# Optimization experiments

Measured on AMD Instinct MI355X. Metric: run time of the kernel, lower is better.

Reference implementation:

```python
import jax, jax.numpy as jnp
import numpy as np

EPS_BN = 1e-5
EPS_LN = 1e-5

def _gelu(x):
    return jax.nn.gelu(x, approximate=False)  # torch nn.GELU default is erf-based

def _conv(x, w, b, stride):
    y = jax.lax.conv_general_dilated(x, w, (stride, stride), 'VALID',
                                     dimension_numbers=('NCHW', 'OIHW', 'NCHW'))
    return y + b[None, :, None, None]

def _bn_train(x, g, b):
    # training-mode BatchNorm2d: batch statistics over (N,H,W), biased variance
    m = x.mean(axis=(0, 2, 3), keepdims=True)
    v = ((x - m) ** 2).mean(axis=(0, 2, 3), keepdims=True)
    return g[None, :, None, None] * (x - m) * jax.lax.rsqrt(v + EPS_BN) + b[None, :, None, None]

def _ln(x, g, b):
    m = x.mean(-1, keepdims=True)
    v = ((x - m) ** 2).mean(-1, keepdims=True)
    return g * (x - m) * jax.lax.rsqrt(v + EPS_LN) + b

def setup_inputs() -> dict:
    key = jax.random.key(0)
    ks = jax.random.split(key, 16)
    B, E, D, H = 1024, 8, 256, 512
    cnn_out = 128 * 14 * 16  # 28672
    s = 0.02
    inp = {
        'x': jax.random.normal(ks[0], (B, 4, 144, 160), jnp.float32),
        'conv1_w': jax.random.normal(ks[1], (32, 4, 8, 8), jnp.float32) * s,
        'conv1_b': jnp.zeros((32,), jnp.float32),
        'bn1_g': jnp.ones((32,), jnp.float32), 'bn1_b': jnp.zeros((32,), jnp.float32),
        'conv2_w': jax.random.normal(ks[2], (64, 32, 4, 4), jnp.float32) * s,
        'conv2_b': jnp.zeros((64,), jnp.float32),
        'bn2_g': jnp.ones((64,), jnp.float32), 'bn2_b': jnp.zeros((64,), jnp.float32),
        'conv3_w': jax.random.normal(ks[3], (128, 64, 3, 3), jnp.float32) * s,
        'conv3_b': jnp.zeros((128,), jnp.float32),
        'bn3_g': jnp.ones((128,), jnp.float32), 'bn3_b': jnp.zeros((128,), jnp.float32),
        'proj_w': jax.random.normal(ks[4], (D, cnn_out), jnp.float32) * 0.005,
        'proj_b': jnp.zeros((D,), jnp.float32),
        'ln_g': jnp.ones((D,), jnp.float32), 'ln_b': jnp.zeros((D,), jnp.float32),
        'router_w': jax.random.normal(ks[5], (E, D), jnp.float32) * 0.01,
        'expert_bias': jnp.zeros((E,), jnp.float32),
        'ew1': jax.random.normal(ks[6], (E, H, D), jnp.float32) * s,
        'eb1': jnp.zeros((E, H), jnp.float32),
        'ew2': jax.random.normal(ks[7], (E, D, H), jnp.float32) * s,
        'eb2': jnp.zeros((E, D), jnp.float32),
        'sw1': jax.random.normal(ks[8], (D, D), jnp.float32) * s,  # shared expert hidden = 512//2 = 256
        'sb1': jnp.zeros((D,), jnp.float32),
        'sw2': jax.random.normal(ks[9], (D, D), jnp.float32) * s,
        'sb2': jnp.zeros((D,), jnp.float32),
        'moe_ln_g': jnp.ones((D,), jnp.float32), 'moe_ln_b': jnp.zeros((D,), jnp.float32),
    }
    return inp

def reference(x, conv1_w, conv1_b, bn1_g, bn1_b, conv2_w, conv2_b, bn2_g, bn2_b,
              conv3_w, conv3_b, bn3_g, bn3_b, proj_w, proj_b, ln_g, ln_b,
              router_w, expert_bias, ew1, eb1, ew2, eb2, sw1, sb1, sw2, sb2,
              moe_ln_g, moe_ln_b):
    B = x.shape[0]
    E = router_w.shape[0]
    top_k = 2
    # conv backbone
    h = _gelu(_bn_train(_conv(x, conv1_w, conv1_b, 4), bn1_g, bn1_b))
    h = _gelu(_bn_train(_conv(h, conv2_w, conv2_b, 2), bn2_g, bn2_b))
    h = _gelu(_bn_train(_conv(h, conv3_w, conv3_b, 1), bn3_g, bn3_b))
    h = h.reshape(B, -1)  # [B, 128*14*16]
    # projection
    h = _gelu(_ln(h @ proj_w.T + proj_b, ln_g, ln_b))  # [B, 256]
    # router (eval: no noise)
    logits = h @ router_w.T + expert_bias          # [B, E]
    probs = jax.nn.softmax(logits, axis=-1)
    wts, idx = jax.lax.top_k(probs, top_k)          # [B, k]
    wts = wts / (wts.sum(-1, keepdims=True) + 1e-8)
    # dense expert compute, sparse combine (same math as masked dispatch loop)
    hid = _gelu(jnp.einsum('bd,ehd->beh', h, ew1) + eb1)   # [B, E, 512]
    eout = jnp.einsum('beh,edh->bed', hid, ew2) + eb2       # [B, E, 256]
    combine = jnp.zeros((B, E), h.dtype).at[jnp.arange(B)[:, None], idx].add(wts)
    out = jnp.einsum('be,bed->bd', combine, eout)
    # shared expert
    shared = _gelu(h @ sw1.T + sb1) @ sw2.T + sb2
    out = out + 0.5 * shared
    # aux losses
    pm = probs.mean(0)
    lb_loss = ((pm - 1.0 / E) ** 2).sum() * E
    z_loss = (logits ** 2).mean() * 0.001
    out = _ln(out, moe_ln_g, moe_ln_b)
    return out, lb_loss, z_loss
```

## Files before the change

kernel.cpp:

```cpp
#include <hip/hip_runtime.h>
#include <hip/hip_bf16.h>
#include <math.h>

typedef unsigned short u16;
typedef unsigned int u32;
typedef __attribute__((ext_vector_type(8))) short bf16x8;
typedef __attribute__((ext_vector_type(4))) float f32x4;

#define DEV __device__ __forceinline__

DEV float gelu_f(float x) { return 0.5f * x * (1.0f + erff(x * 0.70710678118654752f)); }
DEV u16 f2bf(float f) { u32 u = __builtin_bit_cast(u32, f); u = (u + 0x7FFFu + ((u >> 16) & 1u)) >> 16; return (u16)u; }
DEV float bf2f(u16 h) { return __builtin_bit_cast(float, (u32)h << 16); }
DEV u32 fbits(float f) { return __builtin_bit_cast(u32, f); }
DEV float ubits(u32 u) { return __builtin_bit_cast(float, u); }
DEV u32 psplit(float v) {
  u32 u = fbits(v);
  float lo = v - ubits(u & 0xFFFF0000u);
  return (u >> 16) | (fbits(lo) & 0xFFFF0000u);
}
DEV float punp(u32 p) { return ubits(p << 16) + ubits(p & 0xFFFF0000u); }
DEV f32x4 mfma3(bf16x8 ah, bf16x8 al, bf16x8 bh, bf16x8 bl, f32x4 c) {
  c = __builtin_amdgcn_mfma_f32_16x16x32_bf16(al, bh, c, 0, 0, 0);
  c = __builtin_amdgcn_mfma_f32_16x16x32_bf16(ah, bl, c, 0, 0, 0);
  c = __builtin_amdgcn_mfma_f32_16x16x32_bf16(ah, bh, c, 0, 0, 0);
  return c;
}

__global__ void k_zero(float* p, int n) {
  int i = blockIdx.x * blockDim.x + threadIdx.x;
  if (i < n) p[i] = 0.f;
}

__global__ void k_wprep1(const float* __restrict__ w, u16* __restrict__ wh, u16* __restrict__ wl) {
  int idx = blockIdx.x * 256 + threadIdx.x; if (idx >= 8192) return;
  int j = idx & 7, lane = (idx >> 3) & 63, s = (idx >> 9) & 7, oct = idx >> 12;
  int oc = oct * 16 + (lane & 15);
  int kl = ((lane >> 4) << 3) + j;
  int kw = kl >> 2, c = kl & 3, kh = s;
  float v = w[((oc * 4 + c) * 8 + kh) * 8 + kw];
  u16 h = f2bf(v); wh[idx] = h; wl[idx] = f2bf(v - bf2f(h));
}
__global__ void k_wprep2(const float* __restrict__ w, u16* __restrict__ wh, u16* __restrict__ wl) {
  int idx = blockIdx.x * 256 + threadIdx.x; if (idx >= 32768) return;
  int j = idx & 7, lane = (idx >> 3) & 63, s = (idx >> 9) & 15, oct = idx >> 13;
  int oc = oct * 16 + (lane & 15);
  int k = s * 32 + ((lane >> 4) << 3) + j;
  int kh = k >> 7, kw = (k >> 5) & 3, c = k & 31;
  float v = w[((oc * 32 + c) * 4 + kh) * 4 + kw];
  u16 h = f2bf(v); wh[idx] = h; wl[idx] = f2bf(v - bf2f(h));
}
__global__ void k_wprep3(const float* __restrict__ w, u16* __restrict__ wh, u16* __restrict__ wl) {
  int idx = blockIdx.x * 256 + threadIdx.x; if (idx >= 73728) return;
  int j = idx & 7, lane = (idx >> 3) & 63, rest = idx >> 9;
  int s = rest % 18, oct = rest / 18;
  int oc = oct * 16 + (lane & 15);
  int k = s * 32 + ((lane >> 4) << 3) + j;
  int kh = k / 192, r = k - kh * 192;
  int kw = r >> 6, c = r & 63;
  float v = w[((oc * 64 + c) * 3 + kh) * 3 + kw];
  u16 h = f2bf(v); wh[idx] = h; wl[idx] = f2bf(v - bf2f(h));
}
__global__ __launch_bounds__(256) void k_wprepP(const float* __restrict__ w,
    u16* __restrict__ wh, u16* __restrict__ wl)
{
  __shared__ float tile[16][4][225];
  int q = blockIdx.x, oct = blockIdx.y, tid = threadIdx.x;
  for (int i = tid; i < 3584; i += 256) {
    int n = i / 224, rem = i % 224, e = rem / 56, f4 = rem % 56;
    float4 v = *(const float4*)(w + (long)(oct * 16 + n) * 28672 + (4 * q + e) * 224 + f4 * 4);
    tile[n][e][f4 * 4 + 0] = v.x; tile[n][e][f4 * 4 + 1] = v.y;
    tile[n][e][f4 * 4 + 2] = v.z; tile[n][e][f4 * 4 + 3] = v.w;
  }
  __syncthreads();
  int g = (q >> 1) & 3, j0 = 4 * (q & 1), sgb = q >> 3;
  for (int o = tid; o < 3584; o += 256) {
    int pix = o >> 4, ln = o & 15;
    u16 hs[4], ls[4];
#pragma unroll
    for (int e = 0; e < 4; ++e) {
      float v = tile[ln][e][pix];
      u16 h = f2bf(v); hs[e] = h; ls[e] = f2bf(v - bf2f(h));
    }
    long base = (((long)oct * 896 + pix * 4 + sgb) * 64 + g * 16 + ln) * 8 + j0;
    *(uint2*)(wh + base) = make_uint2((u32)hs[0] | ((u32)hs[1] << 16), (u32)hs[2] | ((u32)hs[3] << 16));
    *(uint2*)(wl + base) = make_uint2((u32)ls[0] | ((u32)ls[1] << 16), (u32)ls[2] | ((u32)ls[3] << 16));
  }
}
__global__ void k_wprepG(const float* __restrict__ w, u16* __restrict__ wf,
                         int N, int K, long total)
{
  long idx = (long)blockIdx.x * 256 + threadIdx.x; if (idx >= total) return;
  int j = (int)(idx & 7); int lane = (int)((idx >> 3) & 63); long rest = idx >> 9;
  int kn = K >> 5;
  int s = (int)(rest % kn); long rest2 = rest / kn;
  int noct = N >> 4;
  int oct = (int)(rest2 % noct); int z = (int)(rest2 / noct);
  int n = oct * 16 + (lane & 15);
  int k = s * 32 + ((lane >> 4) << 3) + j;
  wf[idx] = f2bf(w[((long)z * N + n) * K + k]);
}

DEV void c1_store(u16* sin0, u16* sin1, int i, float4 v0, float4 v1) {
  const float* a0 = (const float*)&v0;
  const float* a1 = (const float*)&v1;
  int cp = i / 800, rem = i - cp * 800, r = rem / 40, q = rem - r * 40;
#pragma unroll
  for (int m = 0; m < 4; ++m) {
    float f0 = a0[m], f1 = a1[m];
    u32 u0 = fbits(f0), u1 = fbits(f1);
    u32 hh = (u0 >> 16) | (u1 & 0xFFFF0000u);
    float l0 = f0 - ubits(u0 & 0xFFFF0000u);
    float l1 = f1 - ubits(u1 & 0xFFFF0000u);
    u32 ll = (fbits(l0) >> 16) | (fbits(l1) & 0xFFFF0000u);
    int col = q * 4 + m;
    int idx = r * 320 + col * 2 + cp;
    idx ^= ((col >> 4) & 3) << 2;
    ((u32*)sin0)[idx] = hh;
    ((u32*)sin1)[idx] = ll;
  }
}

__global__ __launch_bounds__(256, 3) void k_conv1m(const float* __restrict__ x,
    const u16* __restrict__ wfh, const u16* __restrict__ wfl,
    const float* __restrict__ bias, u32* __restrict__ y1p, float* __restrict__ sums)
{
  __shared__ __align__(16) u16 sin0[12800], sin1[12800];
  __shared__ float bs1[32], bs2[32];
  int ohp = blockIdx.x, b = blockIdx.y, tid = threadIdx.x;
  int row0 = ohp * 16;
  if (tid < 32) { bs1[tid] = 0.f; bs2[tid] = 0.f; }
  {
    float4 v0r[6], v1r[6];
#pragma unroll
    for (int it = 0; it < 6; ++it) {
      int i = tid + it * 256;
      int cp = i / 800, rem = i - cp * 800, r = rem / 40, q = rem - r * 40;
      int grow = row0 + r;
      float4 z = make_float4(0.f, 0.f, 0.f, 0.f);
      v0r[it] = z; v1r[it] = z;
      if (grow < 144) {
        long base = ((long)b * 4 + 2 * cp) * 23040 + (long)grow * 160 + q * 4;
        v0r[it] = *(const float4*)(x + base);
        v1r[it] = *(const float4*)(x + base + 23040);
      }
    }
#pragma unroll
    for (int it = 0; it < 6; ++it)
      c1_store(sin0, sin1, tid + it * 256, v0r[it], v1r[it]);
    if (tid < 64) {
      int i = 1536 + tid;
      int cp = i / 800, rem = i - cp * 800, r = rem / 40, q = rem - r * 40;
      int grow = row0 + r;
      float4 v0 = make_float4(0.f, 0.f, 0.f, 0.f), v1 = v0;
      if (grow < 144) {
        long base = ((long)b * 4 + 2 * cp) * 23040 + (long)grow * 160 + q * 4;
        v0 = *(const float4*)(x + base);
        v1 = *(const float4*)(x + base + 23040);
      }
      c1_store(sin0, sin1, i, v0, v1);
    }
  }
  __syncthreads();
  int w = tid >> 6, lane = tid & 63, g = lane >> 4, ln = lane & 15;
  int ohls[3], owcs[3];
#pragma unroll
  for (int jj = 0; jj < 3; ++jj) {
    int j = w + 4 * jj;
    ohls[jj] = j / 3;
    int owc = (j % 3) * 16 + ln; if (owc > 38) owc = 38;
    owcs[jj] = owc;
  }
  f32x4 z4 = {0.f, 0.f, 0.f, 0.f};
  f32x4 acc[3][2];
#pragma unroll
  for (int jj = 0; jj < 3; ++jj) { acc[jj][0] = z4; acc[jj][1] = z4; }
#pragma unroll
  for (int kh = 0; kh < 8; ++kh) {
    bf16x8 bh0 = *(const bf16x8*)&wfh[kh * 512 + lane * 8];
    bf16x8 bl0 = *(const bf16x8*)&wfl[kh * 512 + lane * 8];
    bf16x8 bh1 = *(const bf16x8*)&wfh[4096 + kh * 512 + lane * 8];
    bf16x8 bl1 = *(const bf16x8*)&wfl[4096 + kh * 512 + lane * 8];
#pragma unroll
    for (int jj = 0; jj < 3; ++jj) {
      int col = owcs[jj] * 4 + g * 2;
      int off = (4 * ohls[jj] + kh) * 640 + col * 4;
      off ^= ((col >> 4) & 3) << 3;
      bf16x8 ah = *(const bf16x8*)&sin0[off];
      bf16x8 al = *(const bf16x8*)&sin1[off];
      acc[jj][0] = mfma3(ah, al, bh0, bl0, acc[jj][0]);
      acc[jj][1] = mfma3(ah, al, bh1, bl1, acc[jj][1]);
    }
  }
  float s1[2] = {0.f, 0.f}, s2[2] = {0.f, 0.f};
#pragma unroll
  for (int jj = 0; jj < 3; ++jj) {
    int j = w + 4 * jj;
    int ohl = j / 3, owt = j % 3;
    int oh = 4 * ohp + ohl;
    if (oh >= 35) continue;
#pragma unroll
    for (int oct = 0; oct < 2; ++oct) {
      int oc = oct * 16 + ln;
      float bv = bias[oc];
#pragma unroll
      for (int r = 0; r < 4; ++r) {
        int owo = owt * 16 + g * 4 + r;
        if (owo < 39) {
          long oi = ((long)b * 1365 + oh * 39 + owo) * 32 + oc;
          float v = acc[jj][oct][r] + bv;
          y1p[oi] = psplit(v);
          s1[oct] += v; s2[oct] += v * v;
        }
      }
    }
  }
#pragma unroll
  for (int o = 16; o <= 32; o <<= 1) {
    s1[0] += __shfl_xor(s1[0], o); s1[1] += __shfl_xor(s1[1], o);
    s2[0] += __shfl_xor(s2[0], o); s2[1] += __shfl_xor(s2[1], o);
  }
  if (g == 0) {
    atomicAdd(&bs1[ln], s1[0]); atomicAdd(&bs1[16 + ln], s1[1]);
    atomicAdd(&bs2[ln], s2[0]); atomicAdd(&bs2[16 + ln], s2[1]);
  }
  __syncthreads();
  int bkt = b & 7;
  if (tid < 32) {
    atomicAdd(&sums[bkt * 64 + tid], bs1[tid]);
    atomicAdd(&sums[bkt * 64 + 32 + tid], bs2[tid]);
  }
}

DEV void bn_store(u16* sin0, u16* sin1, int i, uint4 p4, int cbmask,
                  const float* sc, const float* shf) {
  int cb = (i & cbmask) * 4;
  u32 hw[2], lw[2];
  u32 pe[4] = { p4.x, p4.y, p4.z, p4.w };
#pragma unroll
  for (int half = 0; half < 2; ++half) {
    float va = punp(pe[half * 2 + 0]);
    float vb = punp(pe[half * 2 + 1]);
    float aa = gelu_f(va * sc[cb + half * 2 + 0] + shf[cb + half * 2 + 0]);
    float ab = gelu_f(vb * sc[cb + half * 2 + 1] + shf[cb + half * 2 + 1]);
    u32 ua = fbits(aa), ub = fbits(ab);
    float la = aa - ubits(ua & 0xFFFF0000u);
    float lb = ab - ubits(ub & 0xFFFF0000u);
    hw[half] = (ua >> 16) | (ub & 0xFFFF0000u);
    lw[half] = (fbits(la) >> 16) | (fbits(lb) & 0xFFFF0000u);
  }
  int iw = i ^ (((i >> 4) & 7) << 1);
  ((uint2*)sin0)[iw] = make_uint2(hw[0], hw[1]);
  ((uint2*)sin1)[iw] = make_uint2(lw[0], lw[1]);
}

__global__ __launch_bounds__(256, 3) void k_conv2m(const u32* __restrict__ y1p,
    const u16* __restrict__ wfh, const u16* __restrict__ wfl,
    const float* __restrict__ scale, const float* __restrict__ shift,
    const float* __restrict__ bias, u32* __restrict__ y2p, float* __restrict__ sums)
{
  __shared__ __align__(16) u16 sin0[12480], sin1[12480];
  __shared__ float sc[32], shf[32];
  __shared__ float bs1[64], bs2[64];
  int ohq = blockIdx.x, b = blockIdx.y, tid = threadIdx.x;
  if (tid < 32) { sc[tid] = scale[tid]; shf[tid] = shift[tid]; }
  if (tid < 64) { bs1[tid] = 0.f; bs2[tid] = 0.f; }
  __syncthreads();
  long sb = ((long)b * 1365 + (long)ohq * 312) * 32;
  const uint4* srcP = (const uint4*)(y1p + sb);
  {
    uint4 pr[12];
#pragma unroll
    for (int it = 0; it < 12; ++it) pr[it] = srcP[tid + it * 256];
#pragma unroll
    for (int it = 0; it < 12; ++it) bn_store(sin0, sin1, tid + it * 256, pr[it], 7, sc, shf);
    if (tid < 48) {
      int i = 3072 + tid;
      bn_store(sin0, sin1, i, srcP[i], 7, sc, shf);
    }
  }
  __syncthreads();
  int w = tid >> 6, lane = tid & 63, g = lane >> 4, ln = lane & 15;
  int oct = w;
  int rowb[5], colb[5];
#pragma unroll
  for (int j = 0; j < 5; ++j) {
    int p = j * 16 + ln; if (p > 71) p = 71;
    int ohl = p / 18, ow = p - 18 * ohl;
    rowb[j] = 2 * ohl; colb[j] = 2 * ow;
  }
  f32x4 z4 = {0.f, 0.f, 0.f, 0.f};
  f32x4 acc[5];
#pragma unroll
  for (int j = 0; j < 5; ++j) acc[j] = z4;
#pragma unroll
  for (int s = 0; s < 16; ++s) {
    int kh = s >> 2, kw = s & 3;
    bf16x8 bh = *(const bf16x8*)&wfh[oct * 8192 + s * 512 + lane * 8];
    bf16x8 bl = *(const bf16x8*)&wfl[oct * 8192 + s * 512 + lane * 8];
#pragma unroll
    for (int j = 0; j < 5; ++j) {
      int colpix = (rowb[j] + kh) * 39 + colb[j] + kw;
      int off = colpix * 32 + g * 8;
      off ^= ((colpix >> 1) & 7) << 3;
      bf16x8 ah = *(const bf16x8*)&sin0[off];
      bf16x8 al = *(const bf16x8*)&sin1[off];
      acc[j] = mfma3(ah, al, bh, bl, acc[j]);
    }
  }
  int oc = oct * 16 + ln;
  float bv = bias[oc];
  float s1 = 0.f, s2 = 0.f;
#pragma unroll
  for (int j = 0; j < 5; ++j) {
#pragma unroll
    for (int r = 0; r < 4; ++r) {
      int po = j * 16 + g * 4 + r;
      if (po < 72) {
        long oi = ((long)b * 288 + (long)ohq * 72 + po) * 64 + oc;
        float v = acc[j][r] + bv;
        y2p[oi] = psplit(v);
        s1 += v; s2 += v * v;
      }
    }
  }
#pragma unroll
  for (int o = 16; o <= 32; o <<= 1) { s1 += __shfl_xor(s1, o); s2 += __shfl_xor(s2, o); }
  if (g == 0) { atomicAdd(&bs1[oc], s1); atomicAdd(&bs2[oc], s2); }
  __syncthreads();
  int bkt = b & 7;
  if (tid < 64) {
    atomicAdd(&sums[bkt * 128 + tid], bs1[tid]);
    atomicAdd(&sums[bkt * 128 + 64 + tid], bs2[tid]);
  }
}

__global__ __launch_bounds__(256, 3) void k_conv3m(const u32* __restrict__ y2p,
    const u16* __restrict__ wfh, const u16* __restrict__ wfl,
    const float* __restrict__ scale, const float* __restrict__ shift,
    const float* __restrict__ bias, u32* __restrict__ y3p, float* __restrict__ sums)
{
  __shared__ __align__(16) u16 sin0[10368], sin1[10368];
  __shared__ float sc[64], shf[64];
  __shared__ float bs1[128], bs2[128];
  int hh = blockIdx.x, b = blockIdx.y, tid = threadIdx.x;
  if (tid < 64) { sc[tid] = scale[tid]; shf[tid] = shift[tid]; }
  if (tid < 128) { bs1[tid] = 0.f; bs2[tid] = 0.f; }
  __syncthreads();
  long sb = ((long)b * 288 + (long)hh * 126) * 64;
  const uint4* srcP = (const uint4*)(y2p + sb);
  {
    uint4 pr[10];
#pragma unroll
    for (int it = 0; it < 10; ++it) pr[it] = srcP[tid + it * 256];
#pragma unroll
    for (int it = 0; it < 10; ++it) bn_store(sin0, sin1, tid + it * 256, pr[it], 15, sc, shf);
    if (tid < 32) {
      int i = 2560 + tid;
      bn_store(sin0, sin1, i, srcP[i], 15, sc, shf);
    }
  }
  __syncthreads();
  int w = tid >> 6, lane = tid & 63, g = lane >> 4, ln = lane & 15;
  int oct0 = w * 2;
  f32x4 z4 = {0.f, 0.f, 0.f, 0.f};
  f32x4 acc[7][2];
#pragma unroll
  for (int j = 0; j < 7; ++j) { acc[j][0] = z4; acc[j][1] = z4; }
#pragma unroll 6
  for (int s = 0; s < 18; ++s) {
    const int kh = s / 6, rm = s % 6;
    const int kw = rm >> 1, ch = rm & 1;
    bf16x8 bh0 = *(const bf16x8*)&wfh[oct0 * 9216 + s * 512 + lane * 8];
    bf16x8 bl0 = *(const bf16x8*)&wfl[oct0 * 9216 + s * 512 + lane * 8];
    bf16x8 bh1 = *(const bf16x8*)&wfh[(oct0 + 1) * 9216 + s * 512 + lane * 8];
    bf16x8 bl1 = *(const bf16x8*)&wfl[(oct0 + 1) * 9216 + s * 512 + lane * 8];
#pragma unroll
    for (int j = 0; j < 7; ++j) {
      int colpix = (j + kh) * 18 + ln + kw;
      int off = colpix * 64 + ch * 32 + g * 8;
      off ^= (colpix & 7) << 3;
      bf16x8 ah = *(const bf16x8*)&sin0[off];
      bf16x8 al = *(const bf16x8*)&sin1[off];
      acc[j][0] = mfma3(ah, al, bh0, bl0, acc[j][0]);
      acc[j][1] = mfma3(ah, al, bh1, bl1, acc[j][1]);
    }
  }
  float s1[2] = {0.f, 0.f}, s2[2] = {0.f, 0.f};
#pragma unroll
  for (int j = 0; j < 7; ++j) {
#pragma unroll
    for (int o2 = 0; o2 < 2; ++o2) {
      int oc = (oct0 + o2) * 16 + ln;
      float bv = bias[oc];
#pragma unroll
      for (int r = 0; r < 4; ++r) {
        int owo = g * 4 + r;
        long oi = ((long)b * 224 + (hh * 7 + j) * 16 + owo) * 128 + oc;
        float v = acc[j][o2][r] + bv;
        y3p[oi] = psplit(v);
        s1[o2] += v; s2[o2] += v * v;
      }
    }
  }
#pragma unroll
  for (int o = 16; o <= 32; o <<= 1) {
    s1[0] += __shfl_xor(s1[0], o); s1[1] += __shfl_xor(s1[1], o);
    s2[0] += __shfl_xor(s2[0], o); s2[1] += __shfl_xor(s2[1], o);
  }
  if (g == 0) {
    atomicAdd(&bs1[oct0 * 16 + ln], s1[0]); atomicAdd(&bs1[(oct0 + 1) * 16 + ln], s1[1]);
    atomicAdd(&bs2[oct0 * 16 + ln], s2[0]); atomicAdd(&bs2[(oct0 + 1) * 16 + ln], s2[1]);
  }
  __syncthreads();
  int bkt = b & 7;
  if (tid < 128) {
    atomicAdd(&sums[bkt * 256 + tid], bs1[tid]);
    atomicAdd(&sums[bkt * 256 + 128 + tid], bs2[tid]);
  }
}

__global__ void k_bn_finalize(const float* __restrict__ sums, const float* __restrict__ g,
    const float* __restrict__ b, float* __restrict__ scale, float* __restrict__ shift,
    int C, float invN)
{
  int c = threadIdx.x;
  if (c < C) {
    float s1 = 0.f, s2 = 0.f;
#pragma unroll
    for (int k = 0; k < 8; ++k) {
      s1 += sums[k * 2 * C + c];
      s2 += sums[k * 2 * C + C + c];
    }
    float m = s1 * invN;
    float var = s2 * invN - m * m;
    float sc = g[c] * rsqrtf(var + 1e-5f);
    scale[c] = sc;
    shift[c] = b[c] - m * sc;
  }
}

__global__ __launch_bounds__(256, 2) void k_projm(const u32* __restrict__ y3p,
    const u16* __restrict__ bh_g, const u16* __restrict__ bl_g,
    const float* __restrict__ scale, const float* __restrict__ shift,
    float* __restrict__ part)
{
  __shared__ __align__(16) u16 Ah[4096], Al[4096];
  __shared__ __align__(16) u16 Bh[8192], Bl[8192];
  __shared__ float sc3[128], sh3[128];
  int m0 = blockIdx.x * 128, by = blockIdx.y, tid = threadIdx.x;
  int w = tid >> 6, lane = tid & 63, g = lane >> 4, ln = lane & 15;
  if (tid < 128) { sc3[tid] = scale[tid]; sh3[tid] = shift[tid]; }
  f32x4 z4 = {0.f, 0.f, 0.f, 0.f};
  f32x4 acc[2][16];
#pragma unroll
  for (int p = 0; p < 2; ++p)
#pragma unroll
    for (int o = 0; o < 16; ++o) acc[p][o] = z4;
  for (int ks = 0; ks < 28; ++ks) {
    __syncthreads();
    long k0 = ((long)by * 28 + ks) * 32;
    int cbase = (int)(k0 & 127);
#pragma unroll
    for (int ii = 0; ii < 4; ++ii) {
      int i = tid + ii * 256;
      int row = i >> 3, q = i & 7;
      uint4 p4 = *((const uint4*)(y3p + (long)(m0 + row) * 28672 + k0) + q);
      u32 pe[4] = { p4.x, p4.y, p4.z, p4.w };
      int c0 = cbase + q * 4;
      u16 hs[4], ls[4];
#pragma unroll
      for (int j = 0; j < 4; ++j) {
        float v = punp(pe[j]);
        float a = gelu_f(v * sc3[c0 + j] + sh3[c0 + j]);
        u32 ua = fbits(a);
        float la = a - ubits(ua & 0xFFFF0000u);
        hs[j] = (u16)(ua >> 16);
        ls[j] = (u16)(fbits(la) >> 16);
      }
      ((uint2*)Ah)[i] = make_uint2((u32)hs[0] | ((u32)hs[1] << 16), (u32)hs[2] | ((u32)hs[3] << 16));
      ((uint2*)Al)[i] = make_uint2((u32)ls[0] | ((u32)ls[1] << 16), (u32)ls[2] | ((u32)ls[3] << 16));
    }
    int ksg = by * 28 + ks;
#pragma unroll
    for (int ii = 0; ii < 8; ++ii) {
      int i = tid + ii * 256;
      int arr = i >> 10, idx = i & 1023, oct = idx >> 6, r2 = idx & 63;
      const u16* src = arr ? bl_g : bh_g;
      u16* dst = arr ? Bl : Bh;
      ((uint4*)dst)[idx] = *((const uint4*)(src + ((long)oct * 896 + ksg) * 512) + r2);
    }
    __syncthreads();
    bf16x8 a_h[2], a_l[2];
#pragma unroll
    for (int pt = 0; pt < 2; ++pt) {
      int off = ((2 * w + pt) * 16 + ln) * 32 + g * 8;
      a_h[pt] = *(const bf16x8*)&Ah[off];
      a_l[pt] = *(const bf16x8*)&Al[off];
    }
#pragma unroll
    for (int oct = 0; oct < 16; ++oct) {
      bf16x8 bh = *(const bf16x8*)&Bh[oct * 512 + lane * 8];
      bf16x8 bl = *(const bf16x8*)&Bl[oct * 512 + lane * 8];
#pragma unroll
      for (int pt = 0; pt < 2; ++pt)
        acc[pt][oct] = mfma3(a_h[pt], a_l[pt], bh, bl, acc[pt][oct]);
    }
  }
#pragma unroll
  for (int pt = 0; pt < 2; ++pt)
#pragma unroll
    for (int oct = 0; oct < 16; ++oct) {
      int oc = oct * 16 + ln;
#pragma unroll
      for (int r = 0; r < 4; ++r) {
        int tok = m0 + (2 * w + pt) * 16 + g * 4 + r;
        part[((long)by * 1024 + tok) * 256 + oc] = acc[pt][oct][r];
      }
    }
}

__global__ __launch_bounds__(256) void k_lnred(const float* __restrict__ part,
    const float* __restrict__ pb, const float* __restrict__ g, const float* __restrict__ be,
    float* __restrict__ h, u16* __restrict__ hb)
{
  int b = blockIdx.x, d = threadIdx.x;
  float s = pb[d];
#pragma unroll
  for (int ks = 0; ks < 32; ++ks) s += part[((long)ks * 1024 + b) * 256 + d];
  __shared__ float red[4];
  float t = s;
  for (int o = 32; o; o >>= 1) t += __shfl_xor(t, o);
  if ((d & 63) == 0) red[d >> 6] = t;
  __syncthreads();
  float mean = (red[0] + red[1] + red[2] + red[3]) * (1.f / 256.f);
  __syncthreads();
  float dv = s - mean;
  t = dv * dv;
  for (int o = 32; o; o >>= 1) t += __shfl_xor(t, o);
  if ((d & 63) == 0) red[d >> 6] = t;
  __syncthreads();
  float var = (red[0] + red[1] + red[2] + red[3]) * (1.f / 256.f);
  float hv = gelu_f(g[d] * dv * rsqrtf(var + 1e-5f) + be[d]);
  h[b * 256 + d] = hv;
  hb[b * 256 + d] = f2bf(hv);
}

__global__ __launch_bounds__(256, 2) void k_gemmb(const u16* __restrict__ A, long aZ, int K,
    const u16* __restrict__ Bf, int noct_tot,
    const float* __restrict__ bias, int biasZ,
    void* __restrict__ C, long cZ, int ldc, int outbf, int act)
{
  __shared__ __align__(16) u16 As[2048];
  __shared__ __align__(16) u16 Bs[8192];
  int m0 = blockIdx.x * 64, nb = blockIdx.y, z = blockIdx.z, tid = threadIdx.x;
  int w = tid >> 6, lane = tid & 63, g = lane >> 4, ln = lane & 15;
  const u16* Az = A + (long)z * aZ;
  int kn = K >> 5;
  f32x4 z4 = {0.f, 0.f, 0.f, 0.f};
  f32x4 acc[16];
#pragma unroll
  for (int o = 0; o < 16; ++o) acc[o] = z4;
  for (int ks = 0; ks < kn; ++ks) {
    __syncthreads();
    {
      int row = tid >> 2, q = tid & 3;
      ((uint4*)As)[tid] = *((const uint4*)(Az + (long)(m0 + row) * K + ks * 32) + q);
    }
#pragma unroll
    for (int ii = 0; ii < 4; ++ii) {
      int i = tid + ii * 256;
      int oct = i >> 6, r2 = i & 63;
      const u16* src = Bf + (((long)z * noct_tot + nb * 16 + oct) * kn + ks) * 512;
      ((uint4*)Bs)[i] = ((const uint4*)src)[r2];
    }
    __syncthreads();
    bf16x8 a = *(const bf16x8*)&As[(w * 16 + ln) * 32 + g * 8];
#pragma unroll
    for (int oct = 0; oct < 16; ++oct) {
      bf16x8 bb = *(const bf16x8*)&Bs[oct * 512 + lane * 8];
      acc[oct] = __builtin_amdgcn_mfma_f32_16x16x32_bf16(a, bb, acc[oct], 0, 0, 0);
    }
  }
#pragma unroll
  for (int oct = 0; oct < 16; ++oct) {
    int n = nb * 256 + oct * 16 + ln;
    float bv = bias[z * biasZ + n];
#pragma unroll
    for (int r = 0; r < 4; ++r) {
      int tok = m0 + w * 16 + g * 4 + r;
      float v = acc[oct][r] + bv;
      if (act) v = gelu_f(v);
      long off = (long)z * cZ + (long)tok * ldc + n;
      if (outbf) ((u16*)C)[off] = f2bf(v);
      else ((float*)C)[off] = v;
    }
  }
}

__global__ __launch_bounds__(64) void k_router(const float* __restrict__ h,
    const float* __restrict__ rw, const float* __restrict__ eb,
    float* __restrict__ wts, int* __restrict__ idx,
    float* __restrict__ pm_sum, float* __restrict__ z_sum)
{
  int b = blockIdx.x, lane = threadIdx.x;
  float4 hv = *(const float4*)(h + b * 256 + lane * 4);
  float logit[8];
#pragma unroll
  for (int e = 0; e < 8; ++e) {
    float4 wv = *(const float4*)(rw + e * 256 + lane * 4);
    float p = hv.x * wv.x + hv.y * wv.y + hv.z * wv.z + hv.w * wv.w;
    for (int o = 32; o; o >>= 1) p += __shfl_xor(p, o);
    logit[e] = p + eb[e];
  }
  float mx = logit[0];
#pragma unroll
  for (int e = 1; e < 8; ++e) mx = fmaxf(mx, logit[e]);
  float pr[8]; float se = 0.f;
#pragma unroll
  for (int e = 0; e < 8; ++e) { pr[e] = expf(logit[e] - mx); se += pr[e]; }
  float inv = 1.f / se;
#pragma unroll
  for (int e = 0; e < 8; ++e) pr[e] *= inv;
  int i0 = 0; float v0 = pr[0];
#pragma unroll
  for (int e = 1; e < 8; ++e) if (pr[e] > v0) { v0 = pr[e]; i0 = e; }
  int i1 = -1; float v1 = -1.f;
#pragma unroll
  for (int e = 0; e < 8; ++e) if (e != i0 && pr[e] > v1) { v1 = pr[e]; i1 = e; }
  if (lane == 0) {
    float ssum = v0 + v1 + 1e-8f;
    wts[2 * b] = v0 / ssum; wts[2 * b + 1] = v1 / ssum;
    idx[2 * b] = i0; idx[2 * b + 1] = i1;
    float zz = 0.f;
#pragma unroll
    for (int e = 0; e < 8; ++e) zz += logit[e] * logit[e];
    atomicAdd(z_sum, zz);
  }
  if (lane < 8) atomicAdd(&pm_sum[lane], pr[lane]);
}

__global__ __launch_bounds__(256) void k_combine_ln(const float* __restrict__ eout,
    const float* __restrict__ sharedB, const float* __restrict__ wts, const int* __restrict__ idx,
    const float* __restrict__ g, const float* __restrict__ bb, float* __restrict__ out)
{
  int b = blockIdx.x, d = threadIdx.x;
  float w0 = wts[2 * b], w1 = wts[2 * b + 1];
  int i0 = idx[2 * b], i1 = idx[2 * b + 1];
  float val = w0 * eout[(long)i0 * 262144 + b * 256 + d]
            + w1 * eout[(long)i1 * 262144 + b * 256 + d]
            + 0.5f * sharedB[b * 256 + d];
  __shared__ float red[4];
  float s = val;
  for (int o = 32; o; o >>= 1) s += __shfl_xor(s, o);
  if ((d & 63) == 0) red[d >> 6] = s;
  __syncthreads();
  float mean = (red[0] + red[1] + red[2] + red[3]) * (1.f / 256.f);
  __syncthreads();
  float dv = val - mean;
  s = dv * dv;
  for (int o = 32; o; o >>= 1) s += __shfl_xor(s, o);
  if ((d & 63) == 0) red[d >> 6] = s;
  __syncthreads();
  float var = (red[0] + red[1] + red[2] + red[3]) * (1.f / 256.f);
  out[b * 256 + d] = g[d] * dv * rsqrtf(var + 1e-5f) + bb[d];
}

__global__ void k_losses(const float* __restrict__ pm_sum, const float* __restrict__ z_sum,
                         float* __restrict__ out)
{
  if (threadIdx.x == 0 && blockIdx.x == 0) {
    float lb = 0.f;
    for (int e = 0; e < 8; ++e) {
      float pm = pm_sum[e] * (1.f / 1024.f);
      float dd = pm - 0.125f;
      lb += dd * dd;
    }
    out[262144] = lb * 8.f;
    out[262145] = z_sum[0] * (1.f / 8192.f) * 0.001f;
  }
}

extern "C" void kernel_launch(void* const* d_in, const int* in_sizes, int n_in,
                              void* d_out, int out_size, void* d_ws, size_t ws_size,
                              hipStream_t stream)
{
  const float* x     = (const float*)d_in[0];
  const float* c1w   = (const float*)d_in[1];
  const float* c1b   = (const float*)d_in[2];
  const float* bn1g  = (const float*)d_in[3];
  const float* bn1b  = (const float*)d_in[4];
  const float* c2w   = (const float*)d_in[5];
  const float* c2b   = (const float*)d_in[6];
  const float* bn2g  = (const float*)d_in[7];
  const float* bn2b  = (const float*)d_in[8];
  const float* c3w   = (const float*)d_in[9];
  const float* c3b   = (const float*)d_in[10];
  const float* bn3g  = (const float*)d_in[11];
  const float* bn3b  = (const float*)d_in[12];
  const float* projw = (const float*)d_in[13];
  const float* projb = (const float*)d_in[14];
  const float* lng   = (const float*)d_in[15];
  const float* lnb   = (const float*)d_in[16];
  const float* rw    = (const float*)d_in[17];
  const float* ebias = (const float*)d_in[18];
  const float* ew1   = (const float*)d_in[19];
  const float* eb1   = (const float*)d_in[20];
  const float* ew2   = (const float*)d_in[21];
  const float* eb2   = (const float*)d_in[22];
  const float* sw1   = (const float*)d_in[23];
  const float* sb1   = (const float*)d_in[24];
  const float* sw2   = (const float*)d_in[25];
  const float* sb2   = (const float*)d_in[26];
  const float* mlng  = (const float*)d_in[27];
  const float* mlnb  = (const float*)d_in[28];
  float* out = (float*)d_out;

  char* W = (char*)d_ws;
  u32* y1p = (u32*)(W + 0);
  u32* y2p = (u32*)(W + 178913280L);
  u32* y3p = (u32*)(W + 0);
  u16* wfph = (u16*)(W + 254410752L);
  u16* wfpl = (u16*)(W + 269090816L);
  u16* wf1h = (u16*)(W + 283770880L);
  u16* wf1l = (u16*)(W + 283787264L);
  u16* wf2h = (u16*)(W + 283803648L);
  u16* wf2l = (u16*)(W + 283869184L);
  u16* wf3h = (u16*)(W + 283934720L);
  u16* wf3l = (u16*)(W + 284082176L);
  float* stats = (float*)(W + 284229632L);
  float* wtsb  = (float*)(W + 284246016L);
  int*   idxb  = (int*)(W + 284254208L);
  float* hbuf  = (float*)(W + 284262400L);
  float* shB   = (float*)(W + 286359552L);
  float* part  = (float*)(W + 178913280L);
  u16* hid     = (u16*)(W + 212467712L);
  u16* ewf1    = (u16*)(W + 220856320L);
  u16* ewf2    = (u16*)(W + 222953472L);
  u16* swf1    = (u16*)(W + 225050624L);
  u16* swf2    = (u16*)(W + 225181696L);
  float* eoutB = (float*)(W + 225312768L);
  u16* hbufb   = (u16*)(W + 233701376L);
  u16* sh1b    = (u16*)(W + 234225664L);

  float* sums1 = stats;
  float* sums2 = stats + 512;
  float* sums3 = stats + 1536;
  float* scale1 = stats + 3584; float* shift1 = stats + 3616;
  float* scale2 = stats + 3648; float* shift2 = stats + 3712;
  float* scale3 = stats + 3776; float* shift3 = stats + 3904;
  float* pm    = stats + 4032;  float* zsum  = stats + 4040;

  dim3 blk(256);
  k_zero<<<dim3(16), blk, 0, stream>>>(stats, 4096);
  k_wprep1<<<dim3(32), blk, 0, stream>>>(c1w, wf1h, wf1l);
  k_wprep2<<<dim3(128), blk, 0, stream>>>(c2w, wf2h, wf2l);
  k_wprep3<<<dim3(288), blk, 0, stream>>>(c3w, wf3h, wf3l);
  k_wprepP<<<dim3(32, 16), blk, 0, stream>>>(projw, wfph, wfpl);

  k_conv1m<<<dim3(9, 1024), blk, 0, stream>>>(x, wf1h, wf1l, c1b, y1p, sums1);
  k_bn_finalize<<<1, 32, 0, stream>>>(sums1, bn1g, bn1b, scale1, shift1, 32, 1.f / 1397760.f);

  k_conv2m<<<dim3(4, 1024), blk, 0, stream>>>(y1p, wf2h, wf2l, scale1, shift1, c2b, y2p, sums2);
  k_bn_finalize<<<1, 64, 0, stream>>>(sums2, bn2g, bn2b, scale2, shift2, 64, 1.f / 294912.f);

  k_conv3m<<<dim3(2, 1024), blk, 0, stream>>>(y2p, wf3h, wf3l, scale2, shift2, c3b, y3p, sums3);
  k_bn_finalize<<<1, 128, 0, stream>>>(sums3, bn3g, bn3b, scale3, shift3, 128, 1.f / 229376.f);

  k_wprepG<<<dim3(4096), blk, 0, stream>>>(ew1, ewf1, 512, 256, 1048576L);
  k_wprepG<<<dim3(4096), blk, 0, stream>>>(ew2, ewf2, 256, 512, 1048576L);
  k_wprepG<<<dim3(256), blk, 0, stream>>>(sw1, swf1, 256, 256, 65536L);
  k_wprepG<<<dim3(256), blk, 0, stream>>>(sw2, swf2, 256, 256, 65536L);

  k_projm<<<dim3(8, 32), blk, 0, stream>>>(y3p, wfph, wfpl, scale3, shift3, part);
  k_lnred<<<dim3(1024), blk, 0, stream>>>(part, projb, lng, lnb, hbuf, hbufb);

  k_router<<<dim3(1024), dim3(64), 0, stream>>>(hbuf, rw, ebias, wtsb, idxb, pm, zsum);

  k_gemmb<<<dim3(16, 2, 8), blk, 0, stream>>>(hbufb, 0L, 256, ewf1, 32, eb1, 512,
                                              (void*)hid, 524288L, 512, 1, 1);
  k_gemmb<<<dim3(16, 1, 8), blk, 0, stream>>>(hid, 524288L, 512, ewf2, 16, eb2, 256,
                                              (void*)eoutB, 262144L, 256, 0, 0);
  k_gemmb<<<dim3(16, 1, 1), blk, 0, stream>>>(hbufb, 0L, 256, swf1, 16, sb1, 0,
                                              (void*)sh1b, 0L, 256, 1, 1);
  k_gemmb<<<dim3(16, 1, 1), blk, 0, stream>>>(sh1b, 0L, 256, swf2, 16, sb2, 0,
                                              (void*)shB, 0L, 256, 0, 0);

  k_combine_ln<<<dim3(1024), blk, 0, stream>>>(eoutB, shB, wtsb, idxb, mlng, mlnb, out);
  k_losses<<<1, 64, 0, stream>>>(pm, zsum, out);
}
```

Before: 712.7 us.

## Merge prep kernels, fold BN finalize into consumers, fuse router and losses

Folds the stats zeroing and all the conv and expert weight-prep kernels into one launch. BN finalize now runs inside each consuming conv or projection block, the router is computed inside the LN-reduce kernel, and the loss kernel is merged into combine_ln. The point is to cut many small kernel launches and the tiny serial gaps between them. In exchange, every block redoes the BN finalize work. The loss tail in combine_ln now reads pm/z sums written by a previous kernel, which stays correct because of stream ordering.

```diff
diff --git a/kernel.cpp b/kernel.cpp
--- a/kernel.cpp
+++ b/kernel.cpp
@@ -26,71 +26,8 @@
   c = __builtin_amdgcn_mfma_f32_16x16x32_bf16(ah, bh, c, 0, 0, 0);
   return c;
 }
-
-__global__ void k_zero(float* p, int n) {
-  int i = blockIdx.x * blockDim.x + threadIdx.x;
-  if (i < n) p[i] = 0.f;
-}
-
-__global__ void k_wprep1(const float* __restrict__ w, u16* __restrict__ wh, u16* __restrict__ wl) {
-  int idx = blockIdx.x * 256 + threadIdx.x; if (idx >= 8192) return;
-  int j = idx & 7, lane = (idx >> 3) & 63, s = (idx >> 9) & 7, oct = idx >> 12;
-  int oc = oct * 16 + (lane & 15);
-  int kl = ((lane >> 4) << 3) + j;
-  int kw = kl >> 2, c = kl & 3, kh = s;
-  float v = w[((oc * 4 + c) * 8 + kh) * 8 + kw];
-  u16 h = f2bf(v); wh[idx] = h; wl[idx] = f2bf(v - bf2f(h));
-}
-__global__ void k_wprep2(const float* __restrict__ w, u16* __restrict__ wh, u16* __restrict__ wl) {
-  int idx = blockIdx.x * 256 + threadIdx.x; if (idx >= 32768) return;
-  int j = idx & 7, lane = (idx >> 3) & 63, s = (idx >> 9) & 15, oct = idx >> 13;
-  int oc = oct * 16 + (lane & 15);
-  int k = s * 32 + ((lane >> 4) << 3) + j;
-  int kh = k >> 7, kw = (k >> 5) & 3, c = k & 31;
-  float v = w[((oc * 32 + c) * 4 + kh) * 4 + kw];
-  u16 h = f2bf(v); wh[idx] = h; wl[idx] = f2bf(v - bf2f(h));
-}
-__global__ void k_wprep3(const float* __restrict__ w, u16* __restrict__ wh, u16* __restrict__ wl) {
-  int idx = blockIdx.x * 256 + threadIdx.x; if (idx >= 73728) return;
-  int j = idx & 7, lane = (idx >> 3) & 63, rest = idx >> 9;
-  int s = rest % 18, oct = rest / 18;
-  int oc = oct * 16 + (lane & 15);
-  int k = s * 32 + ((lane >> 4) << 3) + j;
-  int kh = k / 192, r = k - kh * 192;
-  int kw = r >> 6, c = r & 63;
-  float v = w[((oc * 64 + c) * 3 + kh) * 3 + kw];
-  u16 h = f2bf(v); wh[idx] = h; wl[idx] = f2bf(v - bf2f(h));
-}
-__global__ __launch_bounds__(256) void k_wprepP(const float* __restrict__ w,
-    u16* __restrict__ wh, u16* __restrict__ wl)
-{
-  __shared__ float tile[16][4][225];
-  int q = blockIdx.x, oct = blockIdx.y, tid = threadIdx.x;
-  for (int i = tid; i < 3584; i += 256) {
-    int n = i / 224, rem = i % 224, e = rem / 56, f4 = rem % 56;
-    float4 v = *(const float4*)(w + (long)(oct * 16 + n) * 28672 + (4 * q + e) * 224 + f4 * 4);
-    tile[n][e][f4 * 4 + 0] = v.x; tile[n][e][f4 * 4 + 1] = v.y;
-    tile[n][e][f4 * 4 + 2] = v.z; tile[n][e][f4 * 4 + 3] = v.w;
-  }
-  __syncthreads();
-  int g = (q >> 1) & 3, j0 = 4 * (q & 1), sgb = q >> 3;
-  for (int o = tid; o < 3584; o += 256) {
-    int pix = o >> 4, ln = o & 15;
-    u16 hs[4], ls[4];
-#pragma unroll
-    for (int e = 0; e < 4; ++e) {
-      float v = tile[ln][e][pix];
-      u16 h = f2bf(v); hs[e] = h; ls[e] = f2bf(v - bf2f(h));
-    }
-    long base = (((long)oct * 896 + pix * 4 + sgb) * 64 + g * 16 + ln) * 8 + j0;
-    *(uint2*)(wh + base) = make_uint2((u32)hs[0] | ((u32)hs[1] << 16), (u32)hs[2] | ((u32)hs[3] << 16));
-    *(uint2*)(wl + base) = make_uint2((u32)ls[0] | ((u32)ls[1] << 16), (u32)ls[2] | ((u32)ls[3] << 16));
-  }
-}
-__global__ void k_wprepG(const float* __restrict__ w, u16* __restrict__ wf,
-                         int N, int K, long total)
-{
-  long idx = (long)blockIdx.x * 256 + threadIdx.x; if (idx >= total) return;
+DEV void wprepG_elem(const float* __restrict__ w, u16* __restrict__ wf,
+                     int N, int K, long idx) {
   int j = (int)(idx & 7); int lane = (int)((idx >> 3) & 63); long rest = idx >> 9;
   int kn = K >> 5;
   int s = (int)(rest % kn); long rest2 = rest / kn;
@@ -99,6 +36,91 @@
   int n = oct * 16 + (lane & 15);
   int k = s * 32 + ((lane >> 4) << 3) + j;
   wf[idx] = f2bf(w[((long)z * N + n) * K + k]);
+}
+
+__global__ __launch_bounds__(256) void k_prep(
+    const float* __restrict__ c1w, u16* __restrict__ wf1h, u16* __restrict__ wf1l,
+    const float* __restrict__ c2w, u16* __restrict__ wf2h, u16* __restrict__ wf2l,
+    const float* __restrict__ c3w, u16* __restrict__ wf3h, u16* __restrict__ wf3l,
+    const float* __restrict__ ew1, u16* __restrict__ ewf1,
+    const float* __restrict__ ew2, u16* __restrict__ ewf2,
+    const float* __restrict__ sw1, u16* __restrict__ swf1,
+    const float* __restrict__ sw2, u16* __restrict__ swf2,
+    float* __restrict__ stats)
+{
+  int bx = blockIdx.x, tid = threadIdx.x;
+  if (bx < 16) { int i = bx * 256 + tid; if (i < 4096) stats[i] = 0.f; return; }
+  bx -= 16;
+  if (bx < 32) {
+    int idx = bx * 256 + tid;
+    int j = idx & 7, lane = (idx >> 3) & 63, s = (idx >> 9) & 7, oct = idx >> 12;
+    int oc = oct * 16 + (lane & 15);
+    int kl = ((lane >> 4) << 3) + j;
+    int kw = kl >> 2, c = kl & 3, kh = s;
+    float v = c1w[((oc * 4 + c) * 8 + kh) * 8 + kw];
+    u16 h = f2bf(v); wf1h[idx] = h; wf1l[idx] = f2bf(v - bf2f(h));
+    return;
+  }
+  bx -= 32;
+  if (bx < 128) {
+    int idx = bx * 256 + tid;
+    int j = idx & 7, lane = (idx >> 3) & 63, s = (idx >> 9) & 15, oct = idx >> 13;
+    int oc = oct * 16 + (lane & 15);
+    int k = s * 32 + ((lane >> 4) << 3) + j;
+    int kh = k >> 7, kw = (k >> 5) & 3, c = k & 31;
+    float v = c2w[((oc * 32 + c) * 4 + kh) * 4 + kw];
+    u16 h = f2bf(v); wf2h[idx] = h; wf2l[idx] = f2bf(v - bf2f(h));
+    return;
+  }
+  bx -= 128;
+  if (bx < 288) {
+    int idx = bx * 256 + tid;
+    if (idx >= 73728) return;
+    int j = idx & 7, lane = (idx >> 3) & 63, rest = idx >> 9;
+    int s = rest % 18, oct = rest / 18;
+    int oc = oct * 16 + (lane & 15);
+    int k = s * 32 + ((lane >> 4) << 3) + j;
+    int kh = k / 192, r = k - kh * 192;
+    int kw = r >> 6, c = r & 63;
+    float v = c3w[((oc * 64 + c) * 3 + kh) * 3 + kw];
+    u16 h = f2bf(v); wf3h[idx] = h; wf3l[idx] = f2bf(v - bf2f(h));
+    return;
+  }
+  bx -= 288;
+  if (bx < 4096) { wprepG_elem(ew1, ewf1, 512, 256, (long)bx * 256 + tid); return; }
+  bx -= 4096;
+  if (bx < 4096) { wprepG_elem(ew2, ewf2, 256, 512, (long)bx * 256 + tid); return; }
+  bx -= 4096;
+  if (bx < 256) { wprepG_elem(sw1, swf1, 256, 256, (long)bx * 256 + tid); return; }
+  bx -= 256;
+  wprepG_elem(sw2, swf2, 256, 256, (long)bx * 256 + tid);
+}
+
+__global__ __launch_bounds__(256) void k_wprepP(const float* __restrict__ w,
+    u16* __restrict__ wh, u16* __restrict__ wl)
+{
+  __shared__ float tile[16][4][225];
+  int q = blockIdx.x, oct = blockIdx.y, tid = threadIdx.x;
+  for (int i = tid; i < 3584; i += 256) {
+    int n = i / 224, rem = i % 224, e = rem / 56, f4 = rem % 56;
+    float4 v = *(const float4*)(w + (long)(oct * 16 + n) * 28672 + (4 * q + e) * 224 + f4 * 4);
+    tile[n][e][f4 * 4 + 0] = v.x; tile[n][e][f4 * 4 + 1] = v.y;
+    tile[n][e][f4 * 4 + 2] = v.z; tile[n][e][f4 * 4 + 3] = v.w;
+  }
+  __syncthreads();
+  int g = (q >> 1) & 3, j0 = 4 * (q & 1), sgb = q >> 3;
+  for (int o = tid; o < 3584; o += 256) {
+    int pix = o >> 4, ln = o & 15;
+    u16 hs[4], ls[4];
+#pragma unroll
+    for (int e = 0; e < 4; ++e) {
+      float v = tile[ln][e][pix];
+      u16 h = f2bf(v); hs[e] = h; ls[e] = f2bf(v - bf2f(h));
+    }
+    long base = (((long)oct * 896 + pix * 4 + sgb) * 64 + g * 16 + ln) * 8 + j0;
+    *(uint2*)(wh + base) = make_uint2((u32)hs[0] | ((u32)hs[1] << 16), (u32)hs[2] | ((u32)hs[3] << 16));
+    *(uint2*)(wl + base) = make_uint2((u32)ls[0] | ((u32)ls[1] << 16), (u32)ls[2] | ((u32)ls[3] << 16));
+  }
 }
 
 DEV void c1_store(u16* sin0, u16* sin1, int i, float4 v0, float4 v1) {
@@ -254,16 +276,33 @@
   ((uint2*)sin1)[iw] = make_uint2(lw[0], lw[1]);
 }
 
+DEV void bn_fin(const float* __restrict__ sums, const float* __restrict__ gg,
+                const float* __restrict__ bb, float* sc, float* shf, int C, float invN, int tid) {
+  if (tid < C) {
+    float s1 = 0.f, s2 = 0.f;
+#pragma unroll
+    for (int k = 0; k < 8; ++k) {
+      s1 += sums[k * 2 * C + tid];
+      s2 += sums[k * 2 * C + C + tid];
+    }
+    float m = s1 * invN;
+    float var = s2 * invN - m * m;
+    float scv = gg[tid] * rsqrtf(var + 1e-5f);
+    sc[tid] = scv;
+    shf[tid] = bb[tid] - m * scv;
+  }
+}
+
 __global__ __launch_bounds__(256, 3) void k_conv2m(const u32* __restrict__ y1p,
     const u16* __restrict__ wfh, const u16* __restrict__ wfl,
-    const float* __restrict__ scale, const float* __restrict__ shift,
+    const float* __restrict__ sumsP, const float* __restrict__ bng, const float* __restrict__ bnb,
     const float* __restrict__ bias, u32* __restrict__ y2p, float* __restrict__ sums)
 {
   __shared__ __align__(16) u16 sin0[12480], sin1[12480];
   __shared__ float sc[32], shf[32];
   __shared__ float bs1[64], bs2[64];
   int ohq = blockIdx.x, b = blockIdx.y, tid = threadIdx.x;
-  if (tid < 32) { sc[tid] = scale[tid]; shf[tid] = shift[tid]; }
+  bn_fin(sumsP, bng, bnb, sc, shf, 32, 1.f / 1397760.f, tid);
   if (tid < 64) { bs1[tid] = 0.f; bs2[tid] = 0.f; }
   __syncthreads();
   long sb = ((long)b * 1365 + (long)ohq * 312) * 32;
@@ -337,14 +376,14 @@
 
 __global__ __launch_bounds__(256, 3) void k_conv3m(const u32* __restrict__ y2p,
     const u16* __restrict__ wfh, const u16* __restrict__ wfl,
-    const float* __restrict__ scale, const float* __restrict__ shift,
+    const float* __restrict__ sumsP, const float* __restrict__ bng, const float* __restrict__ bnb,
     const float* __restrict__ bias, u32* __restrict__ y3p, float* __restrict__ sums)
 {
   __shared__ __align__(16) u16 sin0[10368], sin1[10368];
   __shared__ float sc[64], shf[64];
   __shared__ float bs1[128], bs2[128];
   int hh = blockIdx.x, b = blockIdx.y, tid = threadIdx.x;
-  if (tid < 64) { sc[tid] = scale[tid]; shf[tid] = shift[tid]; }
+  bn_fin(sumsP, bng, bnb, sc, shf, 64, 1.f / 294912.f, tid);
   if (tid < 128) { bs1[tid] = 0.f; bs2[tid] = 0.f; }
   __syncthreads();
   long sb = ((long)b * 288 + (long)hh * 126) * 64;
@@ -420,29 +459,9 @@
   }
 }
 
-__global__ void k_bn_finalize(const float* __restrict__ sums, const float* __restrict__ g,
-    const float* __restrict__ b, float* __restrict__ scale, float* __restrict__ shift,
-    int C, float invN)
-{
-  int c = threadIdx.x;
-  if (c < C) {
-    float s1 = 0.f, s2 = 0.f;
-#pragma unroll
-    for (int k = 0; k < 8; ++k) {
-      s1 += sums[k * 2 * C + c];
-      s2 += sums[k * 2 * C + C + c];
-    }
-    float m = s1 * invN;
-    float var = s2 * invN - m * m;
-    float sc = g[c] * rsqrtf(var + 1e-5f);
-    scale[c] = sc;
-    shift[c] = b[c] - m * sc;
-  }
-}
-
 __global__ __launch_bounds__(256, 2) void k_projm(const u32* __restrict__ y3p,
     const u16* __restrict__ bh_g, const u16* __restrict__ bl_g,
-    const float* __restrict__ scale, const float* __restrict__ shift,
+    const float* __restrict__ sumsP, const float* __restrict__ bng, const float* __restrict__ bnb,
     float* __restrict__ part)
 {
   __shared__ __align__(16) u16 Ah[4096], Al[4096];
@@ -450,7 +469,7 @@
   __shared__ float sc3[128], sh3[128];
   int m0 = blockIdx.x * 128, by = blockIdx.y, tid = threadIdx.x;
   int w = tid >> 6, lane = tid & 63, g = lane >> 4, ln = lane & 15;
-  if (tid < 128) { sc3[tid] = scale[tid]; sh3[tid] = shift[tid]; }
+  bn_fin(sumsP, bng, bnb, sc3, sh3, 128, 1.f / 229376.f, tid);
   f32x4 z4 = {0.f, 0.f, 0.f, 0.f};
   f32x4 acc[2][16];
 #pragma unroll
@@ -522,7 +541,9 @@
 
 __global__ __launch_bounds__(256) void k_lnred(const float* __restrict__ part,
     const float* __restrict__ pb, const float* __restrict__ g, const float* __restrict__ be,
-    float* __restrict__ h, u16* __restrict__ hb)
+    const float* __restrict__ rw, const float* __restrict__ eb,
+    u16* __restrict__ hb, float* __restrict__ wts, int* __restrict__ idx,
+    float* __restrict__ pm_sum, float* __restrict__ z_sum)
 {
   int b = blockIdx.x, d = threadIdx.x;
   float s = pb[d];
@@ -542,8 +563,47 @@
   __syncthreads();
   float var = (red[0] + red[1] + red[2] + red[3]) * (1.f / 256.f);
   float hv = gelu_f(g[d] * dv * rsqrtf(var + 1e-5f) + be[d]);
-  h[b * 256 + d] = hv;
   hb[b * 256 + d] = f2bf(hv);
+  __shared__ float lws[8][4];
+  __shared__ float lgs[8];
+  int w = d >> 6;
+#pragma unroll
+  for (int e = 0; e < 8; ++e) {
+    float p = hv * rw[e * 256 + d];
+    for (int o = 32; o; o >>= 1) p += __shfl_xor(p, o);
+    if ((d & 63) == 0) lws[e][w] = p;
+  }
+  __syncthreads();
+  if (d < 8) lgs[d] = lws[d][0] + lws[d][1] + lws[d][2] + lws[d][3] + eb[d];
+  __syncthreads();
+  float logit[8];
+#pragma unroll
+  for (int e = 0; e < 8; ++e) logit[e] = lgs[e];
+  float mx = logit[0];
+#pragma unroll
+  for (int e = 1; e < 8; ++e) mx = fmaxf(mx, logit[e]);
+  float pr[8]; float se = 0.f;
+#pragma unroll
+  for (int e = 0; e < 8; ++e) { pr[e] = expf(logit[e] - mx); se += pr[e]; }
+  float inv = 1.f / se;
+#pragma unroll
+  for (int e = 0; e < 8; ++e) pr[e] *= inv;
+  int i0 = 0; float v0 = pr[0];
+#pragma unroll
+  for (int e = 1; e < 8; ++e) if (pr[e] > v0) { v0 = pr[e]; i0 = e; }
+  int i1 = -1; float v1 = -1.f;
+#pragma unroll
+  for (int e = 0; e < 8; ++e) if (e != i0 && pr[e] > v1) { v1 = pr[e]; i1 = e; }
+  if (d == 0) {
+    float ssum = v0 + v1 + 1e-8f;
+    wts[2 * b] = v0 / ssum; wts[2 * b + 1] = v1 / ssum;
+    idx[2 * b] = i0; idx[2 * b + 1] = i1;
+    float zz = 0.f;
+#pragma unroll
+    for (int e = 0; e < 8; ++e) zz += logit[e] * logit[e];
+    atomicAdd(z_sum, zz);
+  }
+  if (d < 8) atomicAdd(&pm_sum[d], pr[d]);
 }
 
 __global__ __launch_bounds__(256, 2) void k_gemmb(const u16* __restrict__ A, long aZ, int K,
@@ -598,51 +658,10 @@
   }
 }
 
-__global__ __launch_bounds__(64) void k_router(const float* __restrict__ h,
-    const float* __restrict__ rw, const float* __restrict__ eb,
-    float* __restrict__ wts, int* __restrict__ idx,
-    float* __restrict__ pm_sum, float* __restrict__ z_sum)
-{
-  int b = blockIdx.x, lane = threadIdx.x;
-  float4 hv = *(const float4*)(h + b * 256 + lane * 4);
-  float logit[8];
-#pragma unroll
-  for (int e = 0; e < 8; ++e) {
-    float4 wv = *(const float4*)(rw + e * 256 + lane * 4);
-    float p = hv.x * wv.x + hv.y * wv.y + hv.z * wv.z + hv.w * wv.w;
-    for (int o = 32; o; o >>= 1) p += __shfl_xor(p, o);
-    logit[e] = p + eb[e];
-  }
-  float mx = logit[0];
-#pragma unroll
-  for (int e = 1; e < 8; ++e) mx = fmaxf(mx, logit[e]);
-  float pr[8]; float se = 0.f;
-#pragma unroll
-  for (int e = 0; e < 8; ++e) { pr[e] = expf(logit[e] - mx); se += pr[e]; }
-  float inv = 1.f / se;
-#pragma unroll
-  for (int e = 0; e < 8; ++e) pr[e] *= inv;
-  int i0 = 0; float v0 = pr[0];
-#pragma unroll
-  for (int e = 1; e < 8; ++e) if (pr[e] > v0) { v0 = pr[e]; i0 = e; }
-  int i1 = -1; float v1 = -1.f;
-#pragma unroll
-  for (int e = 0; e < 8; ++e) if (e != i0 && pr[e] > v1) { v1 = pr[e]; i1 = e; }
-  if (lane == 0) {
-    float ssum = v0 + v1 + 1e-8f;
-    wts[2 * b] = v0 / ssum; wts[2 * b + 1] = v1 / ssum;
-    idx[2 * b] = i0; idx[2 * b + 1] = i1;
-    float zz = 0.f;
-#pragma unroll
-    for (int e = 0; e < 8; ++e) zz += logit[e] * logit[e];
-    atomicAdd(z_sum, zz);
-  }
-  if (lane < 8) atomicAdd(&pm_sum[lane], pr[lane]);
-}
-
 __global__ __launch_bounds__(256) void k_combine_ln(const float* __restrict__ eout,
     const float* __restrict__ sharedB, const float* __restrict__ wts, const int* __restrict__ idx,
-    const float* __restrict__ g, const float* __restrict__ bb, float* __restrict__ out)
+    const float* __restrict__ g, const float* __restrict__ bb,
+    const float* __restrict__ pm_sum, const float* __restrict__ z_sum, float* __restrict__ out)
 {
   int b = blockIdx.x, d = threadIdx.x;
   float w0 = wts[2 * b], w1 = wts[2 * b + 1];
@@ -664,16 +683,11 @@
   __syncthreads();
   float var = (red[0] + red[1] + red[2] + red[3]) * (1.f / 256.f);
   out[b * 256 + d] = g[d] * dv * rsqrtf(var + 1e-5f) + bb[d];
-}
-
-__global__ void k_losses(const float* __restrict__ pm_sum, const float* __restrict__ z_sum,
-                         float* __restrict__ out)
-{
-  if (threadIdx.x == 0 && blockIdx.x == 0) {
+  if (b == 0 && d == 0) {
     float lb = 0.f;
     for (int e = 0; e < 8; ++e) {
-      float pm = pm_sum[e] * (1.f / 1024.f);
-      float dd = pm - 0.125f;
+      float pmv = pm_sum[e] * (1.f / 1024.f);
+      float dd = pmv - 0.125f;
       lb += dd * dd;
     }
     out[262144] = lb * 8.f;
@@ -731,14 +745,13 @@
   float* stats = (float*)(W + 284229632L);
   float* wtsb  = (float*)(W + 284246016L);
   int*   idxb  = (int*)(W + 284254208L);
-  float* hbuf  = (float*)(W + 284262400L);
   float* shB   = (float*)(W + 286359552L);
+  u16* ewf1    = (u16*)(W + 287408128L);
+  u16* ewf2    = (u16*)(W + 289505280L);
+  u16* swf1    = (u16*)(W + 291602432L);
+  u16* swf2    = (u16*)(W + 291733504L);
   float* part  = (float*)(W + 178913280L);
   u16* hid     = (u16*)(W + 212467712L);
-  u16* ewf1    = (u16*)(W + 220856320L);
-  u16* ewf2    = (u16*)(W + 222953472L);
-  u16* swf1    = (u16*)(W + 225050624L);
-  u16* swf2    = (u16*)(W + 225181696L);
   float* eoutB = (float*)(W + 225312768L);
   u16* hbufb   = (u16*)(W + 233701376L);
   u16* sh1b    = (u16*)(W + 234225664L);
@@ -746,36 +759,21 @@
   float* sums1 = stats;
   float* sums2 = stats + 512;
   float* sums3 = stats + 1536;
-  float* scale1 = stats + 3584; float* shift1 = stats + 3616;
-  float* scale2 = stats + 3648; float* shift2 = stats + 3712;
-  float* scale3 = stats + 3776; float* shift3 = stats + 3904;
   float* pm    = stats + 4032;  float* zsum  = stats + 4040;
 
   dim3 blk(256);
-  k_zero<<<dim3(16), blk, 0, stream>>>(stats, 4096);
-  k_wprep1<<<dim3(32), blk, 0, stream>>>(c1w, wf1h, wf1l);
-  k_wprep2<<<dim3(128), blk, 0, stream>>>(c2w, wf2h, wf2l);
-  k_wprep3<<<dim3(288), blk, 0, stream>>>(c3w, wf3h, wf3l);
+  k_prep<<<dim3(9168), blk, 0, stream>>>(c1w, wf1h, wf1l, c2w, wf2h, wf2l,
+                                         c3w, wf3h, wf3l, ew1, ewf1, ew2, ewf2,
+                                         sw1, swf1, sw2, swf2, stats);
   k_wprepP<<<dim3(32, 16), blk, 0, stream>>>(projw, wfph, wfpl);
 
   k_conv1m<<<dim3(9, 1024), blk, 0, stream>>>(x, wf1h, wf1l, c1b, y1p, sums1);
-  k_bn_finalize<<<1, 32, 0, stream>>>(sums1, bn1g, bn1b, scale1, shift1, 32, 1.f / 1397760.f);
-
-  k_conv2m<<<dim3(4, 1024), blk, 0, stream>>>(y1p, wf2h, wf2l, scale1, shift1, c2b, y2p, sums2);
-  k_bn_finalize<<<1, 64, 0, stream>>>(sums2, bn2g, bn2b, scale2, shift2, 64, 1.f / 294912.f);
-
-  k_conv3m<<<dim3(2, 1024), blk, 0, stream>>>(y2p, wf3h, wf3l, scale2, shift2, c3b, y3p, sums3);
-  k_bn_finalize<<<1, 128, 0, stream>>>(sums3, bn3g, bn3b, scale3, shift3, 128, 1.f / 229376.f);
-
-  k_wprepG<<<dim3(4096), blk, 0, stream>>>(ew1, ewf1, 512, 256, 1048576L);
-  k_wprepG<<<dim3(4096), blk, 0, stream>>>(ew2, ewf2, 256, 512, 1048576L);
-  k_wprepG<<<dim3(256), blk, 0, stream>>>(sw1, swf1, 256, 256, 65536L);
-  k_wprepG<<<dim3(256), blk, 0, stream>>>(sw2, swf2, 256, 256, 65536L);
-
-  k_projm<<<dim3(8, 32), blk, 0, stream>>>(y3p, wfph, wfpl, scale3, shift3, part);
-  k_lnred<<<dim3(1024), blk, 0, stream>>>(part, projb, lng, lnb, hbuf, hbufb);
-
-  k_router<<<dim3(1024), dim3(64), 0, stream>>>(hbuf, rw, ebias, wtsb, idxb, pm, zsum);
+  k_conv2m<<<dim3(4, 1024), blk, 0, stream>>>(y1p, wf2h, wf2l, sums1, bn1g, bn1b, c2b, y2p, sums2);
+  k_conv3m<<<dim3(2, 1024), blk, 0, stream>>>(y2p, wf3h, wf3l, sums2, bn2g, bn2b, c3b, y3p, sums3);
+
+  k_projm<<<dim3(8, 32), blk, 0, stream>>>(y3p, wfph, wfpl, sums3, bn3g, bn3b, part);
+  k_lnred<<<dim3(1024), blk, 0, stream>>>(part, projb, lng, lnb, rw, ebias,
+                                          hbufb, wtsb, idxb, pm, zsum);
 
   k_gemmb<<<dim3(16, 2, 8), blk, 0, stream>>>(hbufb, 0L, 256, ewf1, 32, eb1, 512,
                                               (void*)hid, 524288L, 512, 1, 1);
@@ -786,6 +784,6 @@
   k_gemmb<<<dim3(16, 1, 1), blk, 0, stream>>>(sh1b, 0L, 256, swf2, 16, sb2, 0,
                                               (void*)shB, 0L, 256, 0, 0);
 
-  k_combine_ln<<<dim3(1024), blk, 0, stream>>>(eoutB, shB, wtsb, idxb, mlng, mlnb, out);
-  k_losses<<<1, 64, 0, stream>>>(pm, zsum, out);
-}
+  k_combine_ln<<<dim3(1024), blk, 0, stream>>>(eoutB, shB, wtsb, idxb, mlng, mlnb,
+                                               pm, zsum, out);
+}
```

Measured after the change: 699.5 us (median of 2 runs). About the same (-1.8%).
